# Kernel tuning notes

Hardware: AMD Instinct MI355X
Metric: run time of the kernel (lower is better)

Reference implementation:

```python
import jax, jax.numpy as jnp
import numpy as np

E = 100000   # n_entities
R = 64       # n_relations
I = 256      # in_channels
O = 256      # out_channels
N_EDGES = 1_600_000


def setup_inputs() -> dict:
    key = jax.random.key(0)
    k1, k2, k3, k4 = jax.random.split(key, 4)
    x = jax.random.normal(k1, (E, I), dtype=jnp.float32)
    # cs must be nonzero (it is reciprocated); uniform in [0.5, 1.5)
    cs = jax.random.uniform(k2, (E, R), dtype=jnp.float32) + 0.5
    W = jax.random.normal(k3, (R, I, O), dtype=jnp.float32) * 0.05
    edge_index = jax.random.randint(k4, (2, N_EDGES), 0, E, dtype=jnp.int64)
    return {"x": x, "cs": cs, "W": W, "edge_index": edge_index}


def reference(x, cs, W, edge_index):
    # Faithful to: torch.einsum('er,rio,ej->eo', 1/cs, W, x)
    # i and j are independently contracted indices, so this factorizes:
    # out[e,o] = (sum_j x[e,j]) * sum_r (1/cs[e,r]) * (sum_i W[r,i,o])
    cs_reciprocal = 1.0 / cs                 # (E, R)
    W_sum = jnp.sum(W, axis=1)               # (R, O)
    x_sum = jnp.sum(x, axis=1)               # (E,)
    src = (cs_reciprocal @ W_sum) * x_sum[:, None]  # (E, O)
    return src
```

## Files before the change

### kernel.cpp

```cpp
#include <hip/hip_runtime.h>


constexpr int En = 100000;
constexpr int Rn = 64;
constexpr int In = 256;
constexpr int On = 256;
constexpr int TILES = En / 16;
constexpr int CSP   = 68;

typedef short bf16x8 __attribute__((ext_vector_type(8)));
typedef float floatx4 __attribute__((ext_vector_type(4)));

static __device__ __forceinline__ short f2bf(float f) {
    unsigned u = __builtin_bit_cast(unsigned, f);
    unsigned r = (u + 0x7FFFu + ((u >> 16) & 1u)) >> 16;
    return (short)r;
}

__global__ __launch_bounds__(1024) void wsum_kernel(const float* __restrict__ W,
                                                    short* __restrict__ wsumT) {
    __shared__ float red[16][65];
    const int r  = blockIdx.x >> 2;
    const int h  = blockIdx.x & 3;
    const int ol = threadIdx.x & 63;
    const int ic = threadIdx.x >> 6;
    const int o  = h * 64 + ol;
    const float* base = W + ((size_t)r * In + (size_t)ic * 16) * On + o;
    float s = 0.f;
#pragma unroll
    for (int i = 0; i < 16; ++i) s += base[(size_t)i * On];
    red[ic][ol] = s;
    __syncthreads();
    if (ic == 0) {
        float t = 0.f;
#pragma unroll
        for (int j = 0; j < 16; ++j) t += red[j][ol];
        wsumT[o * Rn + r] = f2bf(t);
    }
}

__global__ __launch_bounds__(256, 4) void out_kernel(const float* __restrict__ x,
                                                     const float* __restrict__ cs,
                                                     const short* __restrict__ wsumT,
                                                     float* __restrict__ out) {
    __shared__ float lds_cs[4][16 * CSP];
    const int wid = (int)threadIdx.x >> 6;
    const int gw  = (int)blockIdx.x * 4 + wid;
    if (gw >= TILES) return;
    const int ln = (int)threadIdx.x & 63;
    const int lm = ln & 15;
    const int q  = ln >> 4;

    const float4* csb = (const float4*)(cs + (size_t)gw * 16 * Rn);
    const float4 cv0 = csb[0 * 64 + ln];
    const float4 cv1 = csb[1 * 64 + ln];
    const float4 cv2 = csb[2 * 64 + ln];
    const float4 cv3 = csb[3 * 64 + ln];

    const float4* xb = (const float4*)(x + (size_t)gw * 16 * In);
    float s[16];
#pragma unroll
    for (int j0 = 0; j0 < 16; j0 += 8) {
        float4 v[8];
#pragma unroll
        for (int j = 0; j < 8; ++j) v[j] = xb[(j0 + j) * 64 + ln];
#pragma unroll
        for (int j = 0; j < 8; ++j) {
            float t = (v[j].x + v[j].y) + (v[j].z + v[j].w);
#pragma unroll
            for (int m = 1; m <= 32; m <<= 1) t += __shfl_xor(t, m, 64);
            s[j0 + j] = t;
        }
    }
    float xs = s[0];
#pragma unroll
    for (int j = 1; j < 16; ++j) xs = (lm == j) ? s[j] : xs;

    {
        float* lw = &lds_cs[wid][(ln >> 4) * CSP + (ln & 15) * 4];
        *(float4*)(lw + 0 * 4 * CSP) = cv0;
        *(float4*)(lw + 1 * 4 * CSP) = cv1;
        *(float4*)(lw + 2 * 4 * CSP) = cv2;
        *(float4*)(lw + 3 * 4 * CSP) = cv3;
    }
    const float* lr = &lds_cs[wid][lm * CSP + q * 8];
    const float4 d0 = *(const float4*)(lr + 0);
    const float4 d1 = *(const float4*)(lr + 4);
    const float4 d2 = *(const float4*)(lr + 32);
    const float4 d3 = *(const float4*)(lr + 36);

    bf16x8 b0, b1;
    {
        const float rv[16] = {d0.x, d0.y, d0.z, d0.w, d1.x, d1.y, d1.z, d1.w,
                              d2.x, d2.y, d2.z, d2.w, d3.x, d3.y, d3.z, d3.w};
#pragma unroll
        for (int j = 0; j < 8; ++j) {
            b0[j] = f2bf(__builtin_amdgcn_rcpf(rv[j]));
            b1[j] = f2bf(__builtin_amdgcn_rcpf(rv[8 + j]));
        }
    }

    float* orow = out + (size_t)(gw * 16 + lm) * On + q * 4;
    const short* wb = wsumT + lm * Rn + q * 8;
#pragma unroll
    for (int ot = 0; ot < 16; ++ot) {
        const short* wp = wb + ot * 16 * Rn;
        const bf16x8 wa0 = *(const bf16x8*)wp;
        const bf16x8 wa1 = *(const bf16x8*)(wp + 32);
        floatx4 acc = {0.f, 0.f, 0.f, 0.f};
        acc = __builtin_amdgcn_mfma_f32_16x16x32_bf16(wa0, b0, acc, 0, 0, 0);
        acc = __builtin_amdgcn_mfma_f32_16x16x32_bf16(wa1, b1, acc, 0, 0, 0);
        const float4 st = make_float4(acc[0] * xs, acc[1] * xs,
                                      acc[2] * xs, acc[3] * xs);
        *(float4*)(orow + ot * 16) = st;
    }
}

extern "C" void kernel_launch(void* const* d_in, const int* in_sizes, int n_in,
                              void* d_out, int out_size, void* d_ws, size_t ws_size,
                              hipStream_t stream) {
    const float* x  = (const float*)d_in[0];
    const float* cs = (const float*)d_in[1];
    const float* W  = (const float*)d_in[2];
    float* out = (float*)d_out;

    short* wsumT = (short*)d_ws;

    wsum_kernel<<<dim3(256), dim3(1024), 0, stream>>>(W, wsumT);
    out_kernel<<<dim3((TILES + 3) / 4), dim3(256), 0, stream>>>(
        x, cs, wsumT, out);
}
```

Before: 238.8 us.

## Make out_kernel persistent with wsum fragments held in registers

Replaces the one-tile-per-wave launch with a fixed grid of 2048 waves that loop over tiles. The bf16 wsum MFMA operands are loaded once per wave into registers and reused for every tile, instead of being reloaded for each tile. Launch bounds drop to 2 blocks per SM to leave room for the extra registers, which lowers occupancy and may reduce latency hiding on a memory-bound kernel.

```diff
diff --git a/kernel.cpp b/kernel.cpp
--- a/kernel.cpp
+++ b/kernel.cpp
@@ -5,8 +5,9 @@
 constexpr int Rn = 64;
 constexpr int In = 256;
 constexpr int On = 256;
-constexpr int TILES = En / 16;
-constexpr int CSP   = 68;
+constexpr int TILES  = En / 16;
+constexpr int CSP    = 68;
+constexpr int NWAVES = 2048;
 
 typedef short bf16x8 __attribute__((ext_vector_type(8)));
 typedef float floatx4 __attribute__((ext_vector_type(4)));
@@ -39,80 +40,86 @@
     }
 }
 
-__global__ __launch_bounds__(256, 4) void out_kernel(const float* __restrict__ x,
+__global__ __launch_bounds__(256, 2) void out_kernel(const float* __restrict__ x,
                                                      const float* __restrict__ cs,
                                                      const short* __restrict__ wsumT,
                                                      float* __restrict__ out) {
     __shared__ float lds_cs[4][16 * CSP];
     const int wid = (int)threadIdx.x >> 6;
     const int gw  = (int)blockIdx.x * 4 + wid;
-    if (gw >= TILES) return;
-    const int ln = (int)threadIdx.x & 63;
-    const int lm = ln & 15;
-    const int q  = ln >> 4;
+    const int ln  = (int)threadIdx.x & 63;
+    const int lm  = ln & 15;
+    const int q   = ln >> 4;
 
-    const float4* csb = (const float4*)(cs + (size_t)gw * 16 * Rn);
-    const float4 cv0 = csb[0 * 64 + ln];
-    const float4 cv1 = csb[1 * 64 + ln];
-    const float4 cv2 = csb[2 * 64 + ln];
-    const float4 cv3 = csb[3 * 64 + ln];
-
-    const float4* xb = (const float4*)(x + (size_t)gw * 16 * In);
-    float s[16];
+    bf16x8 wa0[16], wa1[16];
+    const short* wbase = wsumT + lm * Rn + q * 8;
 #pragma unroll
-    for (int j0 = 0; j0 < 16; j0 += 8) {
-        float4 v[8];
-#pragma unroll
-        for (int j = 0; j < 8; ++j) v[j] = xb[(j0 + j) * 64 + ln];
-#pragma unroll
-        for (int j = 0; j < 8; ++j) {
-            float t = (v[j].x + v[j].y) + (v[j].z + v[j].w);
-#pragma unroll
-            for (int m = 1; m <= 32; m <<= 1) t += __shfl_xor(t, m, 64);
-            s[j0 + j] = t;
-        }
-    }
-    float xs = s[0];
-#pragma unroll
-    for (int j = 1; j < 16; ++j) xs = (lm == j) ? s[j] : xs;
-
-    {
-        float* lw = &lds_cs[wid][(ln >> 4) * CSP + (ln & 15) * 4];
-        *(float4*)(lw + 0 * 4 * CSP) = cv0;
-        *(float4*)(lw + 1 * 4 * CSP) = cv1;
-        *(float4*)(lw + 2 * 4 * CSP) = cv2;
-        *(float4*)(lw + 3 * 4 * CSP) = cv3;
-    }
-    const float* lr = &lds_cs[wid][lm * CSP + q * 8];
-    const float4 d0 = *(const float4*)(lr + 0);
-    const float4 d1 = *(const float4*)(lr + 4);
-    const float4 d2 = *(const float4*)(lr + 32);
-    const float4 d3 = *(const float4*)(lr + 36);
-
-    bf16x8 b0, b1;
-    {
-        const float rv[16] = {d0.x, d0.y, d0.z, d0.w, d1.x, d1.y, d1.z, d1.w,
-                              d2.x, d2.y, d2.z, d2.w, d3.x, d3.y, d3.z, d3.w};
-#pragma unroll
-        for (int j = 0; j < 8; ++j) {
-            b0[j] = f2bf(__builtin_amdgcn_rcpf(rv[j]));
-            b1[j] = f2bf(__builtin_amdgcn_rcpf(rv[8 + j]));
-        }
+    for (int ot = 0; ot < 16; ++ot) {
+        const short* p = wbase + ot * 16 * Rn;
+        wa0[ot] = *(const bf16x8*)p;
+        wa1[ot] = *(const bf16x8*)(p + 32);
     }
 
-    float* orow = out + (size_t)(gw * 16 + lm) * On + q * 4;
-    const short* wb = wsumT + lm * Rn + q * 8;
+    for (int t = gw; t < TILES; t += NWAVES) {
+        const float4* csb = (const float4*)(cs + (size_t)t * 16 * Rn);
+        const float4 cv0 = csb[0 * 64 + ln];
+        const float4 cv1 = csb[1 * 64 + ln];
+        const float4 cv2 = csb[2 * 64 + ln];
+        const float4 cv3 = csb[3 * 64 + ln];
+
+        const float4* xb = (const float4*)(x + (size_t)t * 16 * In);
+        float s[16];
 #pragma unroll
-    for (int ot = 0; ot < 16; ++ot) {
-        const short* wp = wb + ot * 16 * Rn;
-        const bf16x8 wa0 = *(const bf16x8*)wp;
-        const bf16x8 wa1 = *(const bf16x8*)(wp + 32);
-        floatx4 acc = {0.f, 0.f, 0.f, 0.f};
-        acc = __builtin_amdgcn_mfma_f32_16x16x32_bf16(wa0, b0, acc, 0, 0, 0);
-        acc = __builtin_amdgcn_mfma_f32_16x16x32_bf16(wa1, b1, acc, 0, 0, 0);
-        const float4 st = make_float4(acc[0] * xs, acc[1] * xs,
-                                      acc[2] * xs, acc[3] * xs);
-        *(float4*)(orow + ot * 16) = st;
+        for (int j0 = 0; j0 < 16; j0 += 8) {
+            float4 v[8];
+#pragma unroll
+            for (int j = 0; j < 8; ++j) v[j] = xb[(j0 + j) * 64 + ln];
+#pragma unroll
+            for (int j = 0; j < 8; ++j) {
+                float tt = (v[j].x + v[j].y) + (v[j].z + v[j].w);
+#pragma unroll
+                for (int m = 1; m <= 32; m <<= 1) tt += __shfl_xor(tt, m, 64);
+                s[j0 + j] = tt;
+            }
+        }
+        float xs = s[0];
+#pragma unroll
+        for (int j = 1; j < 16; ++j) xs = (lm == j) ? s[j] : xs;
+
+        {
+            float* lw = &lds_cs[wid][(ln >> 4) * CSP + (ln & 15) * 4];
+            *(float4*)(lw + 0 * 4 * CSP) = cv0;
+            *(float4*)(lw + 1 * 4 * CSP) = cv1;
+            *(float4*)(lw + 2 * 4 * CSP) = cv2;
+            *(float4*)(lw + 3 * 4 * CSP) = cv3;
+        }
+        const float* lr = &lds_cs[wid][lm * CSP + q * 8];
+        const float4 d0 = *(const float4*)(lr + 0);
+        const float4 d1 = *(const float4*)(lr + 4);
+        const float4 d2 = *(const float4*)(lr + 32);
+        const float4 d3 = *(const float4*)(lr + 36);
+
+        bf16x8 b0, b1;
+        {
+            const float rv[16] = {d0.x, d0.y, d0.z, d0.w, d1.x, d1.y, d1.z, d1.w,
+                                  d2.x, d2.y, d2.z, d2.w, d3.x, d3.y, d3.z, d3.w};
+#pragma unroll
+            for (int j = 0; j < 8; ++j) {
+                b0[j] = f2bf(__builtin_amdgcn_rcpf(rv[j]));
+                b1[j] = f2bf(__builtin_amdgcn_rcpf(rv[8 + j]));
+            }
+        }
+
+        float* orow = out + (size_t)(t * 16 + lm) * On + q * 4;
+#pragma unroll
+        for (int ot = 0; ot < 16; ++ot) {
+            floatx4 acc = {0.f, 0.f, 0.f, 0.f};
+            acc = __builtin_amdgcn_mfma_f32_16x16x32_bf16(wa0[ot], b0, acc, 0, 0, 0);
+            acc = __builtin_amdgcn_mfma_f32_16x16x32_bf16(wa1[ot], b1, acc, 0, 0, 0);
+            const float4 st = make_float4(acc[0] * xs, acc[1] * xs,
+                                          acc[2] * xs, acc[3] * xs);
+            *(float4*)(orow + ot * 16) = st;
+        }
     }
 }
 
@@ -127,6 +134,6 @@
     short* wsumT = (short*)d_ws;
 
     wsum_kernel<<<dim3(256), dim3(1024), 0, stream>>>(W, wsumT);
-    out_kernel<<<dim3((TILES + 3) / 4), dim3(256), 0, stream>>>(
+    out_kernel<<<dim3(NWAVES / 4), dim3(256), 0, stream>>>(
         x, cs, wsumT, out);
 }
```

Result: no change. 235.7 us (-1.3%).
